# Optimization experiments

Hardware: AMD Instinct MI355X
Metric: run time of the kernel (lower is better)

Reference implementation:

```python
import jax, jax.numpy as jnp
import numpy as np
import math

B, S, D = 2, 2048, 1024
H, HD = 16, 64
ROT = 16          # rotary_dim = head_dim * 0.25
FF = 4096
EPS = 1e-5


def setup_inputs() -> dict:
    key = jax.random.key(0)
    ks = jax.random.split(key, 12)
    sc = lambda *sh: 0.02
    inp = {
        "x": jax.random.normal(ks[0], (B, S, D), jnp.float32),
        "attention_mask": jnp.tril(jnp.ones((S, S), bool))[None, None],  # causal [1,1,S,S]
        "W_qkv": jax.random.normal(ks[1], (3 * D, D), jnp.float32) * 0.02,
        "b_qkv": jnp.zeros((3 * D,), jnp.float32),
        "W_o": jax.random.normal(ks[2], (D, D), jnp.float32) * 0.02,
        "b_o": jnp.zeros((D,), jnp.float32),
        "ln1_w": jnp.ones((D,), jnp.float32),
        "ln1_b": jnp.zeros((D,), jnp.float32),
        "ln2_w": jnp.ones((D,), jnp.float32),
        "ln2_b": jnp.zeros((D,), jnp.float32),
        "W1": jax.random.normal(ks[3], (FF, D), jnp.float32) * 0.02,
        "b1": jnp.zeros((FF,), jnp.float32),
        "W2": jax.random.normal(ks[4], (D, FF), jnp.float32) * 0.02,
        "b2": jnp.zeros((D,), jnp.float32),
    }
    # real rotary frequencies, shaped [1,1,S,ROT//2,2]
    inv_freq = 1.0 / (10000.0 ** (jnp.arange(0, ROT, 2, dtype=jnp.float32) / ROT))
    t = jnp.arange(S, dtype=jnp.float32)
    ang = t[:, None] * inv_freq[None, :]                      # [S, ROT//2]
    inp["freqs_cis"] = jnp.stack([jnp.cos(ang), jnp.sin(ang)], -1)[None, None]
    return inp


def layer_norm(x, w, b):
    mu = jnp.mean(x, -1, keepdims=True)
    var = jnp.mean(jnp.square(x - mu), -1, keepdims=True)
    return (x - mu) * jax.lax.rsqrt(var + EPS) * w + b


def apply_rotate_emb(x, freqs_cis):
    # x: [B,H,S,ROT]; freqs_cis: [1,1,S,ROT//2,2]
    x1, x2 = x[..., : ROT // 2], x[..., ROT // 2 :]
    cos, sin = freqs_cis[..., 0], freqs_cis[..., 1]
    return jnp.concatenate([x1 * cos - x2 * sin, x1 * sin + x2 * cos], -1)


def reference(x, attention_mask, freqs_cis, W_qkv, b_qkv, W_o, b_o,
              ln1_w, ln1_b, ln2_w, ln2_b, W1, b1, W2, b2):
    h = layer_norm(x, ln1_w, ln1_b)
    qkv = jnp.einsum("bsd,ed->bse", h, W_qkv) + b_qkv
    q, k, v = jnp.split(qkv, 3, axis=-1)
    to_heads = lambda t: t.reshape(B, S, H, HD).transpose(0, 2, 1, 3)  # [B,H,S,HD]
    q, k, v = to_heads(q), to_heads(k), to_heads(v)
    q = jnp.concatenate([apply_rotate_emb(q[..., :ROT], freqs_cis), q[..., ROT:]], -1)
    k = jnp.concatenate([apply_rotate_emb(k[..., :ROT], freqs_cis), k[..., ROT:]], -1)
    scores = jnp.einsum("bhqd,bhkd->bhqk", q, k) / math.sqrt(HD)
    scores = jnp.where(attention_mask, scores, -jnp.inf)
    probs = jax.nn.softmax(scores, axis=-1)
    out = jnp.einsum("bhqk,bhkd->bhqd", probs, v)
    out = out.transpose(0, 2, 1, 3).reshape(B, S, D)
    attn_out = jnp.einsum("bsd,ed->bse", out, W_o) + b_o
    # parallel residual (dropout is identity in eval)
    h2 = layer_norm(x, ln2_w, ln2_b)
    ff = jnp.einsum("bsf,df->bsd", jax.nn.gelu(jnp.einsum("bsd,fd->bsf", h2, W1) + b1, approximate=False), W2) + b2
    return x + ff + attn_out
```

## Files before the change

kernel.cpp:

```cpp
#include <hip/hip_runtime.h>

#define DEV __device__ __forceinline__

typedef __bf16 bf16;
typedef bf16 bf16x4 __attribute__((ext_vector_type(4)));
typedef bf16 bf16x8 __attribute__((ext_vector_type(8)));
typedef float f32x4 __attribute__((ext_vector_type(4)));

DEV f32x4 mfma16(bf16x8 a, bf16x8 b, f32x4 c) {
  return __builtin_amdgcn_mfma_f32_16x16x32_bf16(a, b, c, 0, 0, 0);
}

DEV void gload_lds16(const bf16* g, bf16* l) {
  __builtin_amdgcn_global_load_lds((const __attribute__((address_space(1))) void*)g,
                                   (__attribute__((address_space(3))) void*)l, 16, 0, 0);
}

#define PH_BAR __builtin_amdgcn_s_barrier()
#define VM(NSTR) asm volatile("s_waitcnt vmcnt(" NSTR ")" ::: "memory")
#define WAITBAR(NSTR) asm volatile("s_waitcnt vmcnt(" NSTR ")\n\ts_barrier" ::: "memory")

DEV float fast_gelu(float x) {
  const float z = x * x;
  const float w = __builtin_fmaf(z, 0.1029353f, 2.3019853f);
  const float e = __builtin_amdgcn_exp2f(x * w);
  const float r = __builtin_amdgcn_rcpf(1.0f + e);
  return x - x * r;
}

__global__ __launch_bounds__(256) void ln_dual(
    const float* __restrict__ x,
    const float* __restrict__ w1, const float* __restrict__ b1,
    const float* __restrict__ w2, const float* __restrict__ b2,
    bf16* __restrict__ h1, bf16* __restrict__ h2)
{
  __shared__ float red[2][4];
  const int row = blockIdx.x, t = threadIdx.x;
  const int lane = t & 63, wave = t >> 6;
  const float4 v = ((const float4*)(x + (size_t)row * 1024))[t];
  float vv[4] = {v.x, v.y, v.z, v.w};
  float s = vv[0] + vv[1] + vv[2] + vv[3];
  float q = vv[0]*vv[0] + vv[1]*vv[1] + vv[2]*vv[2] + vv[3]*vv[3];
  #pragma unroll
  for (int o = 32; o; o >>= 1) { s += __shfl_xor(s, o); q += __shfl_xor(q, o); }
  if (lane == 0) { red[0][wave] = s; red[1][wave] = q; }
  __syncthreads();
  s = red[0][0] + red[0][1] + red[0][2] + red[0][3];
  q = red[1][0] + red[1][1] + red[1][2] + red[1][3];
  const float mu = s * (1.0f / 1024.0f);
  const float var = q * (1.0f / 1024.0f) - mu * mu;
  const float rs = rsqrtf(var + 1e-5f);
  bf16x4 o1, o2;
  #pragma unroll
  for (int j = 0; j < 4; ++j) {
    const int i = t * 4 + j;
    const float xh = (vv[j] - mu) * rs;
    o1[j] = (bf16)(xh * w1[i] + b1[i]);
    o2[j] = (bf16)(xh * w2[i] + b2[i]);
  }
  *(bf16x4*)&h1[(size_t)row * 1024 + t * 4] = o1;
  *(bf16x4*)&h2[(size_t)row * 1024 + t * 4] = o2;
}

__global__ __launch_bounds__(256) void cast_all(
    const float* __restrict__ Wqkv_f, const float* __restrict__ W1_f,
    const float* __restrict__ Wo_f, const float* __restrict__ W2_f,
    bf16* __restrict__ wQKV, bf16* __restrict__ w1, bf16* __restrict__ wCat)
{
  const int b = blockIdx.x, t = threadIdx.x;
  if (b < 3072) {
    const int i = b * 256 + t;
    const float4 v = ((const float4*)Wqkv_f)[i];
    bf16x4 o = {(bf16)v.x, (bf16)v.y, (bf16)v.z, (bf16)v.w};
    ((bf16x4*)wQKV)[i] = o;
  } else if (b < 7168) {
    const int i = (b - 3072) * 256 + t;
    const float4 v = ((const float4*)W1_f)[i];
    bf16x4 o = {(bf16)v.x, (bf16)v.y, (bf16)v.z, (bf16)v.w};
    ((bf16x4*)w1)[i] = o;
  } else if (b < 8192) {
    const int row = b - 7168;
    const float4 v = *(const float4*)&Wo_f[(size_t)row * 1024 + t * 4];
    bf16x4 o = {(bf16)v.x, (bf16)v.y, (bf16)v.z, (bf16)v.w};
    *(bf16x4*)&wCat[(size_t)row * 5120 + t * 4] = o;
  } else {
    const int row = b - 8192;
    #pragma unroll
    for (int k = 0; k < 4; ++k) {
      const int col = t * 4 + k * 1024;
      const float4 v = *(const float4*)&W2_f[(size_t)row * 4096 + col];
      bf16x4 o = {(bf16)v.x, (bf16)v.y, (bf16)v.z, (bf16)v.w};
      *(bf16x4*)&wCat[(size_t)row * 5120 + 1024 + col] = o;
    }
  }
}

DEV bf16x8 ldfrag(const bf16* unit, int lr, int g) {
  return *(const bf16x8*)&unit[lr * 32 + ((g ^ ((lr >> 1) & 3)) << 3)];
}
DEV void read_bfr(const bf16* unit, int blr, int g, bf16x8 bfr[4]) {
  #pragma unroll
  for (int nj = 0; nj < 4; ++nj) bfr[nj] = ldfrag(unit, blr + nj * 16, g);
}
DEV void read_af(const bf16* unit, int alr, int g, bf16x8 af[4]) {
  #pragma unroll
  for (int ml = 0; ml < 4; ++ml) af[ml] = ldfrag(unit, alr + ml * 16, g);
}
DEV void do_mfma(const bf16x8 af[4], const bf16x8 bfr[4], f32x4 acc[8][4], int mh) {
  __builtin_amdgcn_s_setprio(1);
  #pragma unroll
  for (int ml = 0; ml < 4; ++ml)
    #pragma unroll
    for (int nj = 0; nj < 4; ++nj)
      acc[mh * 4 + ml][nj] = mfma16(af[ml], bfr[nj], acc[mh * 4 + ml][nj]);
  __builtin_amdgcn_s_setprio(0);
}

template <int EPI>
__global__ __launch_bounds__(512) void gemm256(
    const bf16* __restrict__ A, const bf16* __restrict__ B,
    const float* __restrict__ bias, void* __restrict__ Cv,
    float* __restrict__ P1, float* __restrict__ P2, float* __restrict__ P3,
    int K, int ldc, int ntiles, int nbx, int nkt)
{
  __shared__ __align__(16) bf16 As[2][2][2][4096];
  __shared__ __align__(16) bf16 Bs[2][2][2][4096];
  const int tid = threadIdx.x;
  const int lane = tid & 63, wave = tid >> 6;
  const int wm = wave >> 2, wn = wave & 3;
  const int g = lane >> 4, c = lane & 15;
  const int cpx = gridDim.x >> 3;
  const int swz = ((int)blockIdx.x & 7) * cpx + ((int)blockIdx.x >> 3);
  const int tile = swz % ntiles;
  const int sk = swz / ntiles;
  const int bm = (tile / nbx) * 256, bn = (tile % nbx) * 256;

  const int slr = tid >> 2;
  const int sch = (tid & 3) ^ ((tid >> 3) & 3);
  const bf16* aU[2][2];
  const bf16* bU[2][2];
  {
    const bf16* a0 = A + (size_t)(bm + ((slr >> 6) * 128) + (slr & 63)) * K
                       + (size_t)sk * nkt * 64 + sch * 8;
    const bf16* b0 = B + (size_t)(bn + slr) * K + (size_t)sk * nkt * 64 + sch * 8;
    aU[0][0] = a0;            aU[0][1] = a0 + (size_t)64 * K;
    aU[1][0] = a0 + 32;       aU[1][1] = a0 + (size_t)64 * K + 32;
    bU[0][0] = b0;            bU[0][1] = b0 + (size_t)128 * K;
    bU[1][0] = b0 + 32;       bU[1][1] = b0 + (size_t)128 * K + 32;
  }
#define STG_A(bf_, kkh_, ub_, ko_) gload_lds16(aU[kkh_][ub_] + (ko_), &As[bf_][kkh_][ub_][wave * 512])
#define STG_B(bf_, kkh_, ub_, ko_) gload_lds16(bU[kkh_][ub_] + (ko_), &Bs[bf_][kkh_][ub_][wave * 512])

  f32x4 acc[8][4] = {};
  bf16x8 bfr[4], af[4];
  const int alr = (wm << 6) + c;
  const int blr = ((wn & 1) << 6) + c;
  const int bub = wn >> 1;

  STG_B(0, 0, 0, 0); STG_B(0, 0, 1, 0); STG_A(0, 0, 0, 0); STG_A(0, 0, 1, 0);
  STG_B(0, 1, 0, 0); STG_B(0, 1, 1, 0); STG_A(0, 1, 0, 0); STG_A(0, 1, 1, 0);
  WAITBAR("4");

  for (int t = 0; t < nkt - 1; ++t) {
    const int buf = t & 1, nxt = buf ^ 1;
    const int ko = (t + 1) * 64;
    read_bfr(&Bs[buf][0][bub][0], blr, g, bfr);
    read_af(&As[buf][0][0][0], alr, g, af);
    STG_B(nxt, 0, 0, ko); STG_B(nxt, 0, 1, ko);
    PH_BAR;
    do_mfma(af, bfr, acc, 0);
    PH_BAR;
    read_af(&As[buf][0][1][0], alr, g, af);
    STG_A(nxt, 0, 0, ko); STG_A(nxt, 0, 1, ko);
    PH_BAR;
    do_mfma(af, bfr, acc, 1);
    VM("4");
    PH_BAR;
    read_bfr(&Bs[buf][1][bub][0], blr, g, bfr);
    read_af(&As[buf][1][0][0], alr, g, af);
    STG_B(nxt, 1, 0, ko); STG_B(nxt, 1, 1, ko);
    PH_BAR;
    do_mfma(af, bfr, acc, 0);
    PH_BAR;
    read_af(&As[buf][1][1][0], alr, g, af);
    STG_A(nxt, 1, 0, ko); STG_A(nxt, 1, 1, ko);
    PH_BAR;
    do_mfma(af, bfr, acc, 1);
    VM("4");
    PH_BAR;
  }
  {
    const int buf = (nkt - 1) & 1;
    read_bfr(&Bs[buf][0][bub][0], blr, g, bfr);
    read_af(&As[buf][0][0][0], alr, g, af);
    PH_BAR;
    do_mfma(af, bfr, acc, 0);
    PH_BAR;
    read_af(&As[buf][0][1][0], alr, g, af);
    PH_BAR;
    do_mfma(af, bfr, acc, 1);
    VM("0");
    PH_BAR;
    read_bfr(&Bs[buf][1][bub][0], blr, g, bfr);
    read_af(&As[buf][1][0][0], alr, g, af);
    PH_BAR;
    do_mfma(af, bfr, acc, 0);
    PH_BAR;
    read_af(&As[buf][1][1][0], alr, g, af);
    PH_BAR;
    do_mfma(af, bfr, acc, 1);
  }
#undef STG_A
#undef STG_B

  float* Pp = nullptr;
  if constexpr (EPI == 2) Pp = (sk == 1) ? P1 : (sk == 2) ? P2 : (sk == 3) ? P3 : (float*)Cv;
  const int row0 = bm + wm * 128 + 4 * g;
  const int col0 = bn + wn * 64 + c;
  #pragma unroll
  for (int mi = 0; mi < 8; ++mi) {
    #pragma unroll
    for (int nj = 0; nj < 4; ++nj) {
      const int col = col0 + nj * 16;
      float bv = 0.0f;
      if constexpr (EPI < 2) bv = bias[col];
      #pragma unroll
      for (int r = 0; r < 4; ++r) {
        const size_t idx = (size_t)(row0 + mi * 16 + r) * ldc + col;
        float vo = acc[mi][nj][r] + bv;
        if constexpr (EPI == 0) {
          ((bf16*)Cv)[idx] = (bf16)vo;
        } else if constexpr (EPI == 1) {
          ((bf16*)Cv)[idx] = (bf16)fast_gelu(vo);
        } else {
          Pp[idx] = vo;
        }
      }
    }
  }
}

__global__ __launch_bounds__(256) void combine_out(
    const float* __restrict__ p0, const float* __restrict__ p1,
    const float* __restrict__ p2, const float* __restrict__ x,
    const float* __restrict__ bo, const float* __restrict__ b2,
    float* __restrict__ out)
{
  const int row = blockIdx.x, t = threadIdx.x;
  const size_t base = (size_t)row * 1024 + t * 4;
  float4 a = *(float4*)&out[base];
  const float4 v0 = *(const float4*)&p0[base];
  const float4 v1 = *(const float4*)&p1[base];
  const float4 v2 = *(const float4*)&p2[base];
  const float4 vx = *(const float4*)&x[base];
  const float4 vb = *(const float4*)&bo[t * 4];
  const float4 vc = *(const float4*)&b2[t * 4];
  a.x += v0.x + v1.x + v2.x + vx.x + vb.x + vc.x;
  a.y += v0.y + v1.y + v2.y + vx.y + vb.y + vc.y;
  a.z += v0.z + v1.z + v2.z + vx.z + vb.z + vc.z;
  a.w += v0.w + v1.w + v2.w + vx.w + vb.w + vc.w;
  *(float4*)&out[base] = a;
}

__global__ __launch_bounds__(256) void rope_reshape(
    const bf16* __restrict__ qkv, const float* __restrict__ freqs,
    bf16* __restrict__ Q, bf16* __restrict__ K, bf16* __restrict__ VT)
{
  __shared__ bf16 vt[64][72];
  const int t = threadIdx.x;
  const int bh = blockIdx.y, b = bh >> 4, h = bh & 15;
  const int sc = blockIdx.x * 64;
  const int sl = t >> 2, s = sc + sl;
  const int d0 = (t & 3) * 16;

  const size_t rowbase = (size_t)(b * 2048 + s) * 3072 + h * 64 + d0;
  const size_t obase = ((size_t)bh * 2048 + s) * 64 + d0;

  #pragma unroll
  for (int which = 0; which < 2; ++which) {
    const bf16* src = qkv + rowbase + which * 1024;
    bf16x8 v0 = *(const bf16x8*)src;
    bf16x8 v1 = *(const bf16x8*)(src + 8);
    if (d0 == 0) {
      bf16x8 r0, r1;
      #pragma unroll
      for (int j = 0; j < 8; ++j) {
        const float cs = freqs[s * 16 + j * 2];
        const float sn = freqs[s * 16 + j * 2 + 1];
        const float x1 = (float)v0[j], x2 = (float)v1[j];
        r0[j] = (bf16)(x1 * cs - x2 * sn);
        r1[j] = (bf16)(x1 * sn + x2 * cs);
      }
      v0 = r0; v1 = r1;
    }
    bf16* dst = (which == 0 ? Q : K) + obase;
    *(bf16x8*)dst = v0;
    *(bf16x8*)(dst + 8) = v1;
  }
  {
    const bf16* src = qkv + rowbase + 2048;
    bf16x8 v0 = *(const bf16x8*)src;
    bf16x8 v1 = *(const bf16x8*)(src + 8);
    #pragma unroll
    for (int j = 0; j < 8; ++j) { vt[sl][d0 + j] = v0[j]; vt[sl][d0 + 8 + j] = v1[j]; }
  }
  __syncthreads();
  {
    const int d = t >> 2;
    const int s0 = (t & 3) * 16;
    bf16x8 o0, o1;
    #pragma unroll
    for (int j = 0; j < 8; ++j) { o0[j] = vt[s0 + j][d]; o1[j] = vt[s0 + 8 + j][d]; }
    bf16* dst = VT + ((size_t)bh * 64 + d) * 2048 + sc + s0;
    *(bf16x8*)dst = o0;
    *(bf16x8*)(dst + 8) = o1;
  }
}

__global__ __launch_bounds__(512) void attn_kernel(
    const bf16* __restrict__ Q, const bf16* __restrict__ Kg,
    const bf16* __restrict__ VTg, bf16* __restrict__ O, int ldO)
{
  __shared__ __align__(16) bf16 Ks[3][64][64];
  __shared__ __align__(16) bf16 Vs[3][64][64];
  __shared__ __align__(16) bf16 Ps[8][16][64];

  const int tid = threadIdx.x;
  const int lane = tid & 63, wave = tid >> 6;
  const int g = lane >> 4, c = lane & 15;
  const int L = blockIdx.x;
  const int half = L >> 8, r = L & 255;
  const int bh = (half << 4) | (r >> 4);
  const int qtile = half ? (15 - (r & 15)) : (r & 15);
  const int qw = qtile * 128 + wave * 16;

  const bf16* Qp = Q + (size_t)bh * 2048 * 64;
  const bf16* Kp = Kg + (size_t)bh * 2048 * 64;
  const bf16* Vp = VTg + (size_t)bh * 64 * 2048;

  const int srow = lane >> 3;
  const int schunk = (lane & 7) ^ srow;
  const int svr = wave * 8 + srow;
  const size_t kdelta = (size_t)64 * 64;

  bf16x8 qreg[2];
  {
    const float qs = 0.125f * 1.44269504f;
    bf16x8 t0 = *(const bf16x8*)&Qp[(size_t)(qw + c) * 64 + g * 8];
    bf16x8 t1 = *(const bf16x8*)&Qp[(size_t)(qw + c) * 64 + 32 + g * 8];
    #pragma unroll
    for (int j = 0; j < 8; ++j) {
      qreg[0][j] = (bf16)((float)t0[j] * qs);
      qreg[1][j] = (bf16)((float)t1[j] * qs);
    }
  }

  const int cq = c & 7;
  int fo[4][2];
  #pragma unroll
  for (int i = 0; i < 4; ++i)
    #pragma unroll
    for (int kk = 0; kk < 2; ++kk)
      fo[i][kk] = (i * 16 + c) * 64 + (((kk * 4 + g) ^ cq) << 3);
  bf16* pw[4];
  #pragma unroll
  for (int kf = 0; kf < 4; ++kf)
    pw[kf] = &Ps[wave][c][((((kf * 2 + (g >> 1)) ^ cq) << 3)) + ((g & 1) << 2)];
  const bf16* pr[2];
  #pragma unroll
  for (int kk = 0; kk < 2; ++kk)
    pr[kk] = &Ps[wave][c][((kk * 4 + g) ^ cq) << 3];
  const bf16* ks0 = &Ks[0][0][0];
  const bf16* vs0 = &Vs[0][0][0];

  f32x4 oacc[4] = {};
  float m_ = -1e30f, l_ = 0.0f;

  const int nkb = 2 * qtile + 2;
#define STAGE(j_, b3_) do {                                                        \
    gload_lds16(&Kp[(size_t)((j_) * 64 + svr) * 64 + schunk * 8], &Ks[b3_][wave * 8][0]); \
    gload_lds16(&Vp[(size_t)svr * 2048 + (j_) * 64 + schunk * 8], &Vs[b3_][wave * 8][0]); \
  } while (0)

  STAGE(0, 0);
  STAGE(1, 1);
  VM("2");
  PH_BAR;

  for (int kb = 0; kb < nkb; ++kb) {
    const int cur = kb % 3;
    const int kbase = kb * 64;
    const bool more = (kb + 2 < nkb);
    if (more) {
      const int j = kb + 2;
      STAGE(j, j % 3);
    }
    if (kbase <= qw + 15) {
      const bf16* kt = ks0 + cur * kdelta;
      f32x4 st[4] = {};
      __builtin_amdgcn_s_setprio(1);
      #pragma unroll
      for (int kf = 0; kf < 4; ++kf)
        #pragma unroll
        for (int kk = 0; kk < 2; ++kk)
          st[kf] = mfma16(*(const bf16x8*)(kt + fo[kf][kk]), qreg[kk], st[kf]);
      __builtin_amdgcn_s_setprio(0);

      float v[16];
      if (kbase + 63 > qw) {
        const int qrel = qw + c - kbase;
        #pragma unroll
        for (int kf = 0; kf < 4; ++kf)
          #pragma unroll
          for (int rr = 0; rr < 4; ++rr)
            v[kf * 4 + rr] = (kf * 16 + 4 * g + rr <= qrel) ? st[kf][rr] : -1e30f;
      } else {
        #pragma unroll
        for (int kf = 0; kf < 4; ++kf)
          #pragma unroll
          for (int rr = 0; rr < 4; ++rr)
            v[kf * 4 + rr] = st[kf][rr];
      }
      float a0 = fmaxf(v[0], v[1]),  a1 = fmaxf(v[2], v[3]);
      float a2 = fmaxf(v[4], v[5]),  a3 = fmaxf(v[6], v[7]);
      float a4 = fmaxf(v[8], v[9]),  a5 = fmaxf(v[10], v[11]);
      float a6 = fmaxf(v[12], v[13]), a7 = fmaxf(v[14], v[15]);
      float b0 = fmaxf(a0, a1), b1 = fmaxf(a2, a3), b2_ = fmaxf(a4, a5), b3 = fmaxf(a6, a7);
      float tm = fmaxf(fmaxf(b0, b1), fmaxf(b2_, b3));
      tm = fmaxf(tm, __shfl_xor(tm, 16));
      tm = fmaxf(tm, __shfl_xor(tm, 32));
      if (__any(tm > m_ + 8.0f)) {
        const float mn = fmaxf(m_, tm);
        const float alpha = __builtin_amdgcn_exp2f(m_ - mn);
        m_ = mn;
        l_ *= alpha;
        #pragma unroll
        for (int df = 0; df < 4; ++df) {
          oacc[df][0] *= alpha; oacc[df][1] *= alpha;
          oacc[df][2] *= alpha; oacc[df][3] *= alpha;
        }
      }
      float ts = 0.0f;
      bf16 p[16];
      #pragma unroll
      for (int i = 0; i < 16; ++i) {
        const float pv = __builtin_amdgcn_exp2f(v[i] - m_);
        ts += pv;
        p[i] = (bf16)pv;
      }
      ts += __shfl_xor(ts, 16);
      ts += __shfl_xor(ts, 32);
      l_ += ts;
      #pragma unroll
      for (int kf = 0; kf < 4; ++kf) {
        bf16x4 pk = {p[kf * 4], p[kf * 4 + 1], p[kf * 4 + 2], p[kf * 4 + 3]};
        *(bf16x4*)pw[kf] = pk;
      }
      bf16x8 pfrag[2];
      pfrag[0] = *(const bf16x8*)pr[0];
      pfrag[1] = *(const bf16x8*)pr[1];
      const bf16* vt = vs0 + cur * kdelta;
      __builtin_amdgcn_s_setprio(1);
      #pragma unroll
      for (int df = 0; df < 4; ++df)
        #pragma unroll
        for (int kk = 0; kk < 2; ++kk)
          oacc[df] = mfma16(*(const bf16x8*)(vt + fo[df][kk]), pfrag[kk], oacc[df]);
      __builtin_amdgcn_s_setprio(0);
    }
    if (more) { VM("2"); } else { VM("0"); }
    PH_BAR;
  }
#undef STAGE

  const int b = bh >> 4, h = bh & 15;
  const float inv = 1.0f / l_;
  const int s = qw + c;
  #pragma unroll
  for (int df = 0; df < 4; ++df) {
    bf16x4 o;
    #pragma unroll
    for (int rr = 0; rr < 4; ++rr) o[rr] = (bf16)(oacc[df][rr] * inv);
    *(bf16x4*)&O[(size_t)(b * 2048 + s) * ldO + h * 64 + df * 16 + 4 * g] = o;
  }
}

extern "C" void kernel_launch(void* const* d_in, const int* in_sizes, int n_in,
                              void* d_out, int out_size, void* d_ws, size_t ws_size,
                              hipStream_t stream) {
  const float* x     = (const float*)d_in[0];
  const float* W_qkv = (const float*)d_in[2];
  const float* b_qkv = (const float*)d_in[3];
  const float* W_o   = (const float*)d_in[4];
  const float* b_o   = (const float*)d_in[5];
  const float* ln1w  = (const float*)d_in[6];
  const float* ln1b  = (const float*)d_in[7];
  const float* ln2w  = (const float*)d_in[8];
  const float* ln2b  = (const float*)d_in[9];
  const float* W1    = (const float*)d_in[10];
  const float* b1    = (const float*)d_in[11];
  const float* W2    = (const float*)d_in[12];
  const float* b2    = (const float*)d_in[13];
  const float* freqs = (const float*)d_in[14];
  float* out = (float*)d_out;

  char* ws = (char*)d_ws;
  const size_t MB = (size_t)1 << 20;
  bf16* h1   = (bf16*)(ws + 0 * MB);
  bf16* h2   = (bf16*)(ws + 8 * MB);
  bf16* wQKV = (bf16*)(ws + 16 * MB);
  bf16* wCat = (bf16*)(ws + 22 * MB);
  bf16* w1   = (bf16*)(ws + 32 * MB);
  bf16* qkv  = (bf16*)(ws + 40 * MB);
  bf16* Qb   = (bf16*)(ws + 64 * MB);
  bf16* Kb   = (bf16*)(ws + 72 * MB);
  bf16* VTb  = (bf16*)(ws + 80 * MB);
  bf16* A2   = (bf16*)(ws + 88 * MB);
  float* p0  = (float*)(ws + 0 * MB);
  float* p1  = (float*)(ws + 40 * MB);
  float* p2  = (float*)(ws + 64 * MB);

  ln_dual<<<4096, 256, 0, stream>>>(x, ln1w, ln1b, ln2w, ln2b, h1, h2);
  cast_all<<<9216, 256, 0, stream>>>(W_qkv, W1, W_o, W2, wQKV, w1, wCat);

  gemm256<0><<<192, 512, 0, stream>>>(h1, wQKV, b_qkv, qkv,
                                      nullptr, nullptr, nullptr,
                                      1024, 3072, 192, 12, 16);
  rope_reshape<<<dim3(32, 32), 256, 0, stream>>>(qkv, freqs, Qb, Kb, VTb);
  attn_kernel<<<512, 512, 0, stream>>>(Qb, Kb, VTb, A2, 5120);
  gemm256<1><<<256, 512, 0, stream>>>(h2, w1, b1, A2 + 1024,
                                      nullptr, nullptr, nullptr,
                                      1024, 5120, 256, 16, 16);
  gemm256<2><<<256, 512, 0, stream>>>(A2, wCat, nullptr, p0,
                                      p1, p2, out,
                                      5120, 1024, 64, 4, 20);
  combine_out<<<4096, 256, 0, stream>>>(p0, p1, p2, x, b_o, b2, out);
}
```

Measured before the change: 209.6 us.

## Software-pipeline QK^T with softmax-PV and compute row sums via MFMA

Result: no change. 206.0 us (-1.7%).

```diff
diff --git a/kernel.cpp b/kernel.cpp
--- a/kernel.cpp
+++ b/kernel.cpp
@@ -317,7 +317,7 @@
   }
 }
 
-__global__ __launch_bounds__(512) void attn_kernel(
+__global__ __launch_bounds__(512, 4) void attn_kernel(
     const bf16* __restrict__ Q, const bf16* __restrict__ Kg,
     const bf16* __restrict__ VTg, bf16* __restrict__ O, int ldO)
 {
@@ -354,6 +354,9 @@
       qreg[1][j] = (bf16)((float)t1[j] * qs);
     }
   }
+  bf16x8 ones;
+  #pragma unroll
+  for (int j = 0; j < 8; ++j) ones[j] = (bf16)1.0f;
 
   const int cq = c & 7;
   int fo[4][2];
@@ -374,7 +377,8 @@
   const bf16* vs0 = &Vs[0][0][0];
 
   f32x4 oacc[4] = {};
-  float m_ = -1e30f, l_ = 0.0f;
+  f32x4 lacc = {};
+  float m_ = -1e30f;
 
   const int nkb = 2 * qtile + 2;
 #define STAGE(j_, b3_) do {                                                        \
@@ -382,99 +386,102 @@
     gload_lds16(&Vp[(size_t)svr * 2048 + (j_) * 64 + schunk * 8], &Vs[b3_][wave * 8][0]); \
   } while (0)
 
-  STAGE(0, 0);
-  STAGE(1, 1);
-  VM("2");
-  PH_BAR;
-
-  for (int kb = 0; kb < nkb; ++kb) {
-    const int cur = kb % 3;
-    const int kbase = kb * 64;
-    const bool more = (kb + 2 < nkb);
-    if (more) {
-      const int j = kb + 2;
-      STAGE(j, j % 3);
-    }
-    if (kbase <= qw + 15) {
-      const bf16* kt = ks0 + cur * kdelta;
-      f32x4 st[4] = {};
-      __builtin_amdgcn_s_setprio(1);
+  auto qkt = [&](f32x4* st, int bufi) {
+    const bf16* kt = ks0 + bufi * kdelta;
+    __builtin_amdgcn_s_setprio(1);
+    #pragma unroll
+    for (int kf = 0; kf < 4; ++kf) {
+      f32x4 z = {};
+      z = mfma16(*(const bf16x8*)(kt + fo[kf][0]), qreg[0], z);
+      st[kf] = mfma16(*(const bf16x8*)(kt + fo[kf][1]), qreg[1], z);
+    }
+    __builtin_amdgcn_s_setprio(0);
+  };
+
+  auto smpv = [&](const f32x4* st, int j_, int bufi) {
+    const int kbase = j_ * 64;
+    float v[16];
+    if (kbase + 63 > qw) {
+      const int qrel = qw + c - kbase;
       #pragma unroll
       for (int kf = 0; kf < 4; ++kf)
         #pragma unroll
-        for (int kk = 0; kk < 2; ++kk)
-          st[kf] = mfma16(*(const bf16x8*)(kt + fo[kf][kk]), qreg[kk], st[kf]);
-      __builtin_amdgcn_s_setprio(0);
-
-      float v[16];
-      if (kbase + 63 > qw) {
-        const int qrel = qw + c - kbase;
+        for (int rr = 0; rr < 4; ++rr)
+          v[kf * 4 + rr] = (kf * 16 + 4 * g + rr <= qrel) ? st[kf][rr] : -1e30f;
+    } else {
+      #pragma unroll
+      for (int kf = 0; kf < 4; ++kf)
         #pragma unroll
-        for (int kf = 0; kf < 4; ++kf)
-          #pragma unroll
-          for (int rr = 0; rr < 4; ++rr)
-            v[kf * 4 + rr] = (kf * 16 + 4 * g + rr <= qrel) ? st[kf][rr] : -1e30f;
-      } else {
-        #pragma unroll
-        for (int kf = 0; kf < 4; ++kf)
-          #pragma unroll
-          for (int rr = 0; rr < 4; ++rr)
-            v[kf * 4 + rr] = st[kf][rr];
+        for (int rr = 0; rr < 4; ++rr)
+          v[kf * 4 + rr] = st[kf][rr];
+    }
+    float u0 = fmaxf(fmaxf(v[0], v[1]), v[2]);
+    float u1 = fmaxf(fmaxf(v[3], v[4]), v[5]);
+    float u2 = fmaxf(fmaxf(v[6], v[7]), v[8]);
+    float u3 = fmaxf(fmaxf(v[9], v[10]), v[11]);
+    float u4 = fmaxf(fmaxf(v[12], v[13]), v[14]);
+    float tm = fmaxf(fmaxf(fmaxf(u0, u1), u2), fmaxf(fmaxf(u3, u4), v[15]));
+    if (__any(tm > m_ + 8.0f)) {
+      float tr = fmaxf(tm, __shfl_xor(tm, 16));
+      tr = fmaxf(tr, __shfl_xor(tr, 32));
+      const float mn = fmaxf(m_, tr);
+      const float alpha = __builtin_amdgcn_exp2f(m_ - mn);
+      m_ = mn;
+      lacc[0] *= alpha; lacc[1] *= alpha; lacc[2] *= alpha; lacc[3] *= alpha;
+      #pragma unroll
+      for (int df = 0; df < 4; ++df) {
+        oacc[df][0] *= alpha; oacc[df][1] *= alpha;
+        oacc[df][2] *= alpha; oacc[df][3] *= alpha;
       }
-      float a0 = fmaxf(v[0], v[1]),  a1 = fmaxf(v[2], v[3]);
-      float a2 = fmaxf(v[4], v[5]),  a3 = fmaxf(v[6], v[7]);
-      float a4 = fmaxf(v[8], v[9]),  a5 = fmaxf(v[10], v[11]);
-      float a6 = fmaxf(v[12], v[13]), a7 = fmaxf(v[14], v[15]);
-      float b0 = fmaxf(a0, a1), b1 = fmaxf(a2, a3), b2_ = fmaxf(a4, a5), b3 = fmaxf(a6, a7);
-      float tm = fmaxf(fmaxf(b0, b1), fmaxf(b2_, b3));
-      tm = fmaxf(tm, __shfl_xor(tm, 16));
-      tm = fmaxf(tm, __shfl_xor(tm, 32));
-      if (__any(tm > m_ + 8.0f)) {
-        const float mn = fmaxf(m_, tm);
-        const float alpha = __builtin_amdgcn_exp2f(m_ - mn);
-        m_ = mn;
-        l_ *= alpha;
-        #pragma unroll
-        for (int df = 0; df < 4; ++df) {
-          oacc[df][0] *= alpha; oacc[df][1] *= alpha;
-          oacc[df][2] *= alpha; oacc[df][3] *= alpha;
-        }
-      }
-      float ts = 0.0f;
-      bf16 p[16];
-      #pragma unroll
-      for (int i = 0; i < 16; ++i) {
-        const float pv = __builtin_amdgcn_exp2f(v[i] - m_);
-        ts += pv;
-        p[i] = (bf16)pv;
-      }
-      ts += __shfl_xor(ts, 16);
-      ts += __shfl_xor(ts, 32);
-      l_ += ts;
-      #pragma unroll
-      for (int kf = 0; kf < 4; ++kf) {
-        bf16x4 pk = {p[kf * 4], p[kf * 4 + 1], p[kf * 4 + 2], p[kf * 4 + 3]};
-        *(bf16x4*)pw[kf] = pk;
-      }
-      bf16x8 pfrag[2];
-      pfrag[0] = *(const bf16x8*)pr[0];
-      pfrag[1] = *(const bf16x8*)pr[1];
-      const bf16* vt = vs0 + cur * kdelta;
-      __builtin_amdgcn_s_setprio(1);
-      #pragma unroll
-      for (int df = 0; df < 4; ++df)
-        #pragma unroll
-        for (int kk = 0; kk < 2; ++kk)
-          oacc[df] = mfma16(*(const bf16x8*)(vt + fo[df][kk]), pfrag[kk], oacc[df]);
-      __builtin_amdgcn_s_setprio(0);
-    }
-    if (more) { VM("2"); } else { VM("0"); }
+    }
+    bf16 p[16];
+    #pragma unroll
+    for (int i = 0; i < 16; ++i)
+      p[i] = (bf16)__builtin_amdgcn_exp2f(v[i] - m_);
+    #pragma unroll
+    for (int kf = 0; kf < 4; ++kf) {
+      bf16x4 pk = {p[kf * 4], p[kf * 4 + 1], p[kf * 4 + 2], p[kf * 4 + 3]};
+      *(bf16x4*)pw[kf] = pk;
+    }
+    bf16x8 pfrag0 = *(const bf16x8*)pr[0];
+    bf16x8 pfrag1 = *(const bf16x8*)pr[1];
+    const bf16* vt = vs0 + bufi * kdelta;
+    __builtin_amdgcn_s_setprio(1);
+    #pragma unroll
+    for (int df = 0; df < 4; ++df) {
+      oacc[df] = mfma16(*(const bf16x8*)(vt + fo[df][0]), pfrag0, oacc[df]);
+      oacc[df] = mfma16(*(const bf16x8*)(vt + fo[df][1]), pfrag1, oacc[df]);
+    }
+    lacc = mfma16(ones, pfrag0, lacc);
+    lacc = mfma16(ones, pfrag1, lacc);
+    __builtin_amdgcn_s_setprio(0);
+  };
+
+  f32x4 stA[4], stB[4];
+  STAGE(0, 0);
+  STAGE(1, 1);
+  VM("0");
+  PH_BAR;
+  qkt(stA, 0);
+
+  const int nit = nkb >> 1;
+  for (int i = 0; i < nit; ++i) {
+    const int jA = 2 * i, jB = 2 * i + 1;
+    if (jA + 2 < nkb) STAGE(jA + 2, (jA + 2) % 3);
+    if (jB * 64 <= qw + 15) qkt(stB, jB % 3);
+    if (jA * 64 <= qw + 15) smpv(stA, jA, jA % 3);
+    VM("0");
+    PH_BAR;
+    if (jB + 2 < nkb) STAGE(jB + 2, (jB + 2) % 3);
+    if (jB + 1 < nkb && (jB + 1) * 64 <= qw + 15) qkt(stA, (jB + 1) % 3);
+    if (jB * 64 <= qw + 15) smpv(stB, jB, jB % 3);
+    VM("0");
     PH_BAR;
   }
 #undef STAGE
 
   const int b = bh >> 4, h = bh & 15;
-  const float inv = 1.0f / l_;
+  const float inv = 1.0f / lacc[0];
   const int s = qw + c;
   #pragma unroll
   for (int df = 0; df < 4; ++df) {
```
